# Kernel tuning notes

Hardware: AMD Instinct MI355X
Metric: run time of the kernel (lower is better)

Reference implementation:

```python
import jax, jax.numpy as jnp
import numpy as np
import math

N_EMBD = 1024
N_HEAD = 16
B, T = 4, 2048

def setup_inputs() -> dict:
    key = jax.random.key(0)
    k1, k2, k3, k4, k5 = jax.random.split(key, 5)
    C = N_EMBD
    scale_in = 1.0 / math.sqrt(C)
    x = jax.random.normal(k1, (B, T, C), dtype=jnp.float32)
    W_attn = jax.random.normal(k2, (C, 3 * C), dtype=jnp.float32) * scale_in
    b_attn = jax.random.normal(k3, (3 * C,), dtype=jnp.float32) * 0.02
    W_proj = jax.random.normal(k4, (C, C), dtype=jnp.float32) * scale_in
    b_proj = jax.random.normal(k5, (C,), dtype=jnp.float32) * 0.02
    attention_mask = jnp.ones((B, T), dtype=jnp.int32)
    return {"x": x, "W_attn": W_attn, "b_attn": b_attn,
            "W_proj": W_proj, "b_proj": b_proj,
            "attention_mask": attention_mask}

def reference(x, W_attn, b_attn, W_proj, b_proj, attention_mask):
    Bx, Tx, C = x.shape
    H = N_HEAD
    D = C // H
    qkv = x @ W_attn + b_attn                      # [B,T,3C]
    q, k, v = jnp.split(qkv, 3, axis=-1)
    # [B,H,T,D]
    q = q.reshape(Bx, Tx, H, D).transpose(0, 2, 1, 3)
    k = k.reshape(Bx, Tx, H, D).transpose(0, 2, 1, 3)
    v = v.reshape(Bx, Tx, H, D).transpose(0, 2, 1, 3)
    att = jnp.einsum('bhqd,bhkd->bhqk', q, k) * (1.0 / math.sqrt(D))
    causal = jnp.tril(jnp.ones((Tx, Tx), dtype=bool))  # [T,T]
    neg_inf = jnp.float32(-jnp.inf)
    att = jnp.where(causal[None, None, :, :], att, neg_inf)
    pad = (attention_mask != 0)[:, None, None, :]      # [B,1,1,T]
    att = jnp.where(pad, att, neg_inf)
    att = jax.nn.softmax(att, axis=-1)
    y = jnp.einsum('bhqk,bhkd->bhqd', att, v)          # [B,H,T,D]
    y = y.transpose(0, 2, 1, 3).reshape(Bx, Tx, C)
    y = y @ W_proj + b_proj
    return y
```

## Files before the change

### kernel.cpp

```cpp
#include <hip/hip_runtime.h>
#include <hip/hip_bf16.h>
#include <stdint.h>

#define B_ 4
#define T_ 2048
#define C_ 1024
#define H_ 16
#define D_ 64
#define BH_ (B_*H_)
#define M_ (B_*T_)

typedef __attribute__((ext_vector_type(8))) short short8;
typedef __attribute__((ext_vector_type(4))) float f32x4;
typedef __attribute__((ext_vector_type(16))) float f32x16;

#if __has_builtin(__builtin_amdgcn_exp2f)
#define EXP2(x) __builtin_amdgcn_exp2f(x)
#else
#define EXP2(x) exp2f(x)
#endif

#define QSCALE 0.18033688011112043f

__device__ __forceinline__ unsigned short f2bf(float f) {
  union { float f; unsigned int u; } v; v.f = f;
  unsigned int r = v.u + 0x7FFFu + ((v.u >> 16) & 1u);
  return (unsigned short)(r >> 16);
}

__device__ __forceinline__ unsigned int cvtpk_bf16(float lo, float hi) {
  unsigned int r;
  asm("v_cvt_pk_bf16_f32 %0, %1, %2" : "=v"(r) : "v"(lo), "v"(hi));
  return r;
}

__device__ __forceinline__ void gload_lds16(const void* g, void* l) {
  __builtin_amdgcn_global_load_lds(
      (__attribute__((address_space(1))) void*)g,
      (__attribute__((address_space(3))) void*)l, 16, 0, 0);
}

__global__ __launch_bounds__(256) void k_cvt(const float* __restrict__ in,
                                             unsigned short* __restrict__ out, int n) {
  int i = (blockIdx.x * 256 + threadIdx.x) * 4;
  if (i >= n) return;
  float4 v = *reinterpret_cast<const float4*>(in + i);
  union { unsigned short u[4]; unsigned long long ll; } o;
  o.u[0] = f2bf(v.x); o.u[1] = f2bf(v.y); o.u[2] = f2bf(v.z); o.u[3] = f2bf(v.w);
  *reinterpret_cast<unsigned long long*>(out + i) = o.ll;
}

__global__ __launch_bounds__(256) void k_tr(const float* __restrict__ W,
                                            unsigned short* __restrict__ Wt, int K, int N) {
  __shared__ float t[32][33];
  int n0 = blockIdx.x * 32, k0 = blockIdx.y * 32;
  int tx = threadIdx.x, ty = threadIdx.y;
  #pragma unroll
  for (int j = 0; j < 4; j++)
    t[ty + j*8][tx] = W[(size_t)(k0 + ty + j*8) * N + n0 + tx];
  __syncthreads();
  #pragma unroll
  for (int j = 0; j < 4; j++)
    Wt[(size_t)(n0 + ty + j*8) * K + k0 + tx] = f2bf(t[tx][ty + j*8]);
}

template<int QKV>
__global__ __launch_bounds__(256) void k_gemm4(const unsigned short* __restrict__ A,
                                               const unsigned short* __restrict__ Bt,
                                               const float* __restrict__ bias,
                                               void* __restrict__ outp, int N, int K) {
  __shared__ __align__(16) unsigned short Al[2][128*64];
  __shared__ __align__(16) unsigned short Bl[2][128*64];

  const int tid = threadIdx.x;
  const int lane = tid & 63, wv = tid >> 6;
  const int lg = lane >> 4, lr = lane & 15;
  const int wm = wv >> 1, wn = wv & 1;

  const int nwg = gridDim.x * gridDim.y;
  const int l = blockIdx.y * gridDim.x + blockIdx.x;
  const int wg = (l & 7) * (nwg >> 3) + (l >> 3);
  const int m0 = (wg / gridDim.x) * 128;
  const int n0 = (wg % gridDim.x) * 128;

  const int NT = K >> 6;

  auto stageA = [&](int s, int t) {
    #pragma unroll
    for (int u = 0; u < 4; ++u) {
      int gi = tid + u*256;
      int row = gi >> 3, g = gi & 7;
      gload_lds16(A + (size_t)(m0 + row) * K + t*64 + (g ^ (row & 7)) * 8,
                  (char*)Al[s] + gi*16);
    }
  };
  auto stageB = [&](int s, int t) {
    #pragma unroll
    for (int u = 0; u < 4; ++u) {
      int gi = tid + u*256;
      int row = gi >> 3, g = gi & 7;
      gload_lds16(Bt + (size_t)(n0 + row) * K + t*64 + (g ^ (row & 7)) * 8,
                  (char*)Bl[s] + gi*16);
    }
  };

  f32x4 acc[4][4];
  #pragma unroll
  for (int i = 0; i < 4; ++i)
    #pragma unroll
    for (int j = 0; j < 4; ++j) acc[i][j] = (f32x4){0.f, 0.f, 0.f, 0.f};

  stageA(0, 0); stageB(0, 0);
  asm volatile("s_waitcnt vmcnt(0)" ::: "memory");
  __builtin_amdgcn_s_barrier();

  for (int t = 0; t < NT; ++t) {
    const char* Asb = (const char*)Al[t & 1];
    const char* Bsb = (const char*)Bl[t & 1];
    const int s1 = (t & 1) ^ 1;
    const bool sn = (t + 1 < NT);
    short8 af[2][2], ag[2][2], bf[4][2];

    #pragma unroll
    for (int mf = 0; mf < 2; ++mf) {
      int row = wm*64 + mf*16 + lr; int r7 = row & 7;
      af[mf][0] = *(const short8*)(Asb + row*128 + ((lg      ^ r7) << 4));
      af[mf][1] = *(const short8*)(Asb + row*128 + (((4|lg) ^ r7) << 4));
    }
    #pragma unroll
    for (int nf = 0; nf < 4; ++nf) {
      int col = wn*64 + nf*16 + lr; int c7 = col & 7;
      bf[nf][0] = *(const short8*)(Bsb + col*128 + ((lg      ^ c7) << 4));
      bf[nf][1] = *(const short8*)(Bsb + col*128 + (((4|lg) ^ c7) << 4));
    }
    if (sn) { stageA(s1, t + 1); stageB(s1, t + 1); }
    __builtin_amdgcn_s_barrier();
    asm volatile("s_waitcnt lgkmcnt(0)" ::: "memory");
    __builtin_amdgcn_sched_barrier(0);
    __builtin_amdgcn_s_setprio(1);
    #pragma unroll
    for (int kh = 0; kh < 2; ++kh)
      #pragma unroll
      for (int mf = 0; mf < 2; ++mf)
        #pragma unroll
        for (int nf = 0; nf < 4; ++nf)
          acc[mf][nf] = __builtin_amdgcn_mfma_f32_16x16x32_bf16(
              af[mf][kh], bf[nf][kh], acc[mf][nf], 0, 0, 0);
    __builtin_amdgcn_s_setprio(0);
    __builtin_amdgcn_s_barrier();

    #pragma unroll
    for (int mf = 0; mf < 2; ++mf) {
      int row = wm*64 + (mf+2)*16 + lr; int r7 = row & 7;
      ag[mf][0] = *(const short8*)(Asb + row*128 + ((lg      ^ r7) << 4));
      ag[mf][1] = *(const short8*)(Asb + row*128 + (((4|lg) ^ r7) << 4));
    }
    __builtin_amdgcn_s_barrier();
    asm volatile("s_waitcnt lgkmcnt(0)" ::: "memory");
    __builtin_amdgcn_sched_barrier(0);
    __builtin_amdgcn_s_setprio(1);
    #pragma unroll
    for (int kh = 0; kh < 2; ++kh)
      #pragma unroll
      for (int mf = 0; mf < 2; ++mf)
        #pragma unroll
        for (int nf = 0; nf < 4; ++nf)
          acc[mf+2][nf] = __builtin_amdgcn_mfma_f32_16x16x32_bf16(
              ag[mf][kh], bf[nf][kh], acc[mf+2][nf], 0, 0, 0);
    __builtin_amdgcn_s_setprio(0);
    asm volatile("s_waitcnt vmcnt(0)" ::: "memory");
    __builtin_amdgcn_s_barrier();
  }

  if (QKV) {
    unsigned short* qb = (unsigned short*)outp;
    const size_t SZ = (size_t)BH_ * T_ * D_;
    #pragma unroll
    for (int i4 = 0; i4 < 4; ++i4) {
      int mb = m0 + wm*64 + i4*16 + lg*4;
      #pragma unroll
      for (int nf = 0; nf < 4; ++nf) {
        int n = n0 + wn*64 + nf*16 + lr;
        float bv = bias[n];
        int which = n >> 10, c = n & 1023, h = c >> 6, d = c & 63;
        if (which == 2) {
          int bb2 = mb >> 11, tt = mb & 2047;
          union { unsigned short h4[4]; unsigned long long ll; } pk;
          #pragma unroll
          for (int r = 0; r < 4; ++r) pk.h4[r] = f2bf(acc[i4][nf][r] + bv);
          unsigned short* vbase = qb + 2 * SZ;
          *reinterpret_cast<unsigned long long*>(
              &vbase[((size_t)(bb2*H_ + h)*D_ + d)*T_ + tt]) = pk.ll;
        } else {
          unsigned short* base = qb + (size_t)which * SZ;
          #pragma unroll
          for (int r = 0; r < 4; ++r) {
            int m = mb + r;
            int bb2 = m >> 11, tt = m & 2047;
            float y = acc[i4][nf][r] + bv;
            if (which == 0) y *= QSCALE;
            base[((size_t)(bb2*H_ + h)*T_ + tt)*D_ + d] = f2bf(y);
          }
        }
      }
    }
  } else {
    float* out = (float*)outp;
    #pragma unroll
    for (int i4 = 0; i4 < 4; ++i4) {
      int mb = m0 + wm*64 + i4*16 + lg*4;
      #pragma unroll
      for (int nf = 0; nf < 4; ++nf) {
        int n = n0 + wn*64 + nf*16 + lr;
        float bv = bias[n];
        #pragma unroll
        for (int r = 0; r < 4; ++r)
          out[(size_t)(mb + r)*N + n] = acc[i4][nf][r] + bv;
      }
    }
  }
}

__global__ __launch_bounds__(256, 2) void k_attn4(const unsigned short* __restrict__ Qb,
                                                  const unsigned short* __restrict__ Kb,
                                                  const unsigned short* __restrict__ Vb,
                                                  const int* __restrict__ amask,
                                                  unsigned short* __restrict__ Yb) {
  __shared__ __align__(16) char pool[65536];

  const int l = blockIdx.y * 16 + blockIdx.x;
  const int local = l >> 3;
  const int tq = 15 - (local >> 3);
  const int bh = (l & 7) * 8 + (local & 7);
  const int bb = bh >> 4, hh = bh & 15;

  const int tid = threadIdx.x;
  const int lane = tid & 63, w = tid >> 6;
  const int hi = lane >> 5, l31 = lane & 31;

  const unsigned short* Qh = Qb + (size_t)bh * (T_*D_);
  const unsigned short* Kh = Kb + (size_t)bh * (T_*D_);
  const unsigned short* Vh = Vb + (size_t)bh * (T_*D_);

  auto stage_load = [&](int i, int b, int& nm0, int& nm1) {
    const int kv0 = i << 7;
    char* base = pool + b * 32768;
    #pragma unroll
    for (int s = 0; s < 4; ++s) {
      int gi = tid + s * 256;
      int row = gi >> 3, gc = gi & 7;
      gload_lds16(Kh + (size_t)(kv0 + row)*D_ + (gc ^ (row & 7)) * 8, base + gi * 16);
    }
    #pragma unroll
    for (int s = 0; s < 4; ++s) {
      int gi = tid + s * 256;
      int d = gi >> 4, q = gi & 15;
      gload_lds16(Vh + (size_t)d*T_ + kv0 + ((q ^ (d & 15)) * 8),
                  base + 16384 + gi * 16);
    }
    nm0 = amask[bb*T_ + kv0 + lane];
    nm1 = amask[bb*T_ + kv0 + 64 + lane];
  };

  const int nT = tq + 1;
  const int qbase = tq << 7;
  const int qw = qbase + w * 32;
  const int q  = qw + l31;

  short8 qf[4];
  #pragma unroll
  for (int dt = 0; dt < 4; ++dt)
    qf[dt] = *reinterpret_cast<const short8*>(Qh + (size_t)q*D_ + dt*16 + hi*8);

  f32x16 o0, o1;
  #pragma unroll
  for (int r = 0; r < 16; ++r) { o0[r] = 0.f; o1[r] = 0.f; }
  float mr = 0.f, ls = 0.f;

  int cm0, cm1;
  stage_load(0, 0, cm0, cm1);
  __syncthreads();

  for (int i = 0; i < nT; ++i) {
    const int b = i & 1;
    const bool pf = (i + 1 < nT);
    int nm0 = 0, nm1 = 0;
    if (pf) stage_load(i + 1, b ^ 1, nm0, nm1);
    const int kv0 = i << 7;

    const unsigned short* Klb = (const unsigned short*)(pool + b * 32768);
    const char* Vtb = pool + b * 32768 + 16384;

    f32x16 st[4];
    #pragma unroll
    for (int tl = 0; tl < 4; ++tl)
      #pragma unroll
      for (int r = 0; r < 16; ++r) st[tl][r] = 0.f;
    __builtin_amdgcn_s_setprio(1);
    #pragma unroll
    for (int dt = 0; dt < 4; ++dt) {
      int gg = dt * 2 + hi;
      #pragma unroll
      for (int tl = 0; tl < 4; ++tl) {
        int ra = tl*32 + l31;
        short8 kf = *reinterpret_cast<const short8*>(Klb + ra*64 + ((gg ^ (ra & 7)) * 8));
        st[tl] = __builtin_amdgcn_mfma_f32_32x32x16_bf16(kf, qf[dt], st[tl], 0, 0, 0);
      }
    }
    __builtin_amdgcn_s_setprio(0);

    if (kv0 + 127 > qw) {
      #pragma unroll
      for (int tl = 0; tl < 4; ++tl)
        #pragma unroll
        for (int r = 0; r < 16; ++r) {
          int kvl = tl*32 + (r & 3) + 8 * (r >> 2) + 4 * hi;
          if (kv0 + kvl > q) st[tl][r] = -1e30f;
        }
    }
    unsigned long long mb0 = __ballot(cm0 != 0);
    unsigned long long mb1 = __ballot(cm1 != 0);
    if ((mb0 & mb1) != ~0ull) {
      #pragma unroll
      for (int tl = 0; tl < 4; ++tl) {
        unsigned long long mb = (tl < 2) ? mb0 : mb1;
        int sh0 = (tl & 1) * 32;
        #pragma unroll
        for (int r = 0; r < 16; ++r) {
          int kvl = (r & 3) + 8 * (r >> 2) + 4 * hi;
          if (!((mb >> (kvl + sh0)) & 1)) st[tl][r] = -1e30f;
        }
      }
    }

    float rp[8];
    #pragma unroll
    for (int r = 0; r < 8; ++r) rp[r] = 0.f;
    #pragma unroll
    for (int tl = 0; tl < 4; ++tl)
      #pragma unroll
      for (int r = 0; r < 16; ++r) {
        st[tl][r] = EXP2(st[tl][r] - mr);
        rp[r & 7] += st[tl][r];
      }
    float rs = ((rp[0] + rp[1]) + (rp[2] + rp[3])) + ((rp[4] + rp[5]) + (rp[6] + rp[7]));
    rs += __shfl_xor(rs, 32);

    unsigned int pw[4][4][2];
    #pragma unroll
    for (int tl = 0; tl < 4; ++tl)
      #pragma unroll
      for (int a = 0; a < 4; ++a) {
        pw[tl][a][0] = cvtpk_bf16(st[tl][4*a],   st[tl][4*a+1]);
        pw[tl][a][1] = cvtpk_bf16(st[tl][4*a+2], st[tl][4*a+3]);
      }

    #pragma unroll
    for (int kt = 0; kt < 8; ++kt) {
      const int t = kt >> 1, h2 = kt & 1;
      unsigned int send0 = hi ? pw[t][2*h2][0]   : pw[t][2*h2+1][0];
      unsigned int send1 = hi ? pw[t][2*h2][1]   : pw[t][2*h2+1][1];
      unsigned int own0  = hi ? pw[t][2*h2+1][0] : pw[t][2*h2][0];
      unsigned int own1  = hi ? pw[t][2*h2+1][1] : pw[t][2*h2][1];
      unsigned int recv0 = __shfl_xor(send0, 32);
      unsigned int recv1 = __shfl_xor(send1, 32);
      union { unsigned int u[4]; short8 v; } pf2;
      pf2.u[0] = hi ? recv0 : own0;
      pf2.u[1] = hi ? recv1 : own1;
      pf2.u[2] = hi ? own0  : recv0;
      pf2.u[3] = hi ? own1  : recv1;
      int gg = kt * 2 + hi;
      int dA = l31;
      short8 vf0 = *reinterpret_cast<const short8*>(Vtb + dA*256 + ((gg ^ (dA & 15)) * 16));
      int dB = 32 + l31;
      short8 vf1 = *reinterpret_cast<const short8*>(Vtb + dB*256 + ((gg ^ (dB & 15)) * 16));
      __builtin_amdgcn_s_setprio(1);
      o0 = __builtin_amdgcn_mfma_f32_32x32x16_bf16(vf0, pf2.v, o0, 0, 0, 0);
      o1 = __builtin_amdgcn_mfma_f32_32x32x16_bf16(vf1, pf2.v, o1, 0, 0, 0);
      __builtin_amdgcn_s_setprio(0);
    }

    if (__all(rs <= 65536.f)) {
      ls += rs;
    } else {
      float lgf;
      asm("v_log_f32 %0, %1" : "=v"(lgf) : "v"(rs));
      int lgi = (int)lgf + 1;
      float corr = __int_as_float((unsigned)(127 - lgi) << 23);
      mr += (float)lgi;
      ls = (ls + rs) * corr;
      #pragma unroll
      for (int r = 0; r < 16; ++r) { o0[r] *= corr; o1[r] *= corr; }
    }

    if (pf) { cm0 = nm0; cm1 = nm1; }
    __syncthreads();
  }

  float inv = 1.0f / ls;
  size_t rowbase = ((size_t)bb*T_ + q)*C_ + hh*D_;
  #pragma unroll
  for (int a = 0; a < 4; ++a) {
    union { unsigned short h[4]; unsigned long long ll; } y0, y1;
    #pragma unroll
    for (int bq = 0; bq < 4; ++bq) {
      int r = 4*a + bq;
      y0.h[bq] = f2bf(o0[r] * inv);
      y1.h[bq] = f2bf(o1[r] * inv);
    }
    int d0o = 8*a + 4*hi;
    *reinterpret_cast<unsigned long long*>(Yb + rowbase + d0o)      = y0.ll;
    *reinterpret_cast<unsigned long long*>(Yb + rowbase + 32 + d0o) = y1.ll;
  }
}

extern "C" void kernel_launch(void* const* d_in, const int* in_sizes, int n_in,
                              void* d_out, int out_size, void* d_ws, size_t ws_size,
                              hipStream_t stream) {
  const float* x      = (const float*)d_in[0];
  const float* W_attn = (const float*)d_in[1];
  const float* b_attn = (const float*)d_in[2];
  const float* W_proj = (const float*)d_in[3];
  const float* b_proj = (const float*)d_in[4];
  const int*   amask  = (const int*)d_in[5];
  float* out = (float*)d_out;

  char* ws = (char*)d_ws;
  size_t off = 0;
  auto alloc = [&](size_t bytes) { char* p = ws + off; off += (bytes + 255) & ~(size_t)255; return p; };
  unsigned short* xb   = (unsigned short*)alloc((size_t)M_ * C_ * 2);
  unsigned short* Wta  = (unsigned short*)alloc((size_t)3 * C_ * C_ * 2);
  unsigned short* Wtp  = (unsigned short*)alloc((size_t)C_ * C_ * 2);
  unsigned short* qkvb = (unsigned short*)alloc((size_t)3 * BH_ * T_ * D_ * 2);
  unsigned short* Yb   = (unsigned short*)alloc((size_t)M_ * C_ * 2);

  k_cvt<<<(M_ * C_) / 1024, 256, 0, stream>>>(x, xb, M_ * C_);
  k_tr<<<dim3(3*C_/32, C_/32), dim3(32, 8), 0, stream>>>(W_attn, Wta, C_, 3*C_);
  k_tr<<<dim3(C_/32,  C_/32),  dim3(32, 8), 0, stream>>>(W_proj, Wtp, C_, C_);

  k_gemm4<1><<<dim3(3*C_/128, M_/128), 256, 0, stream>>>(xb, Wta, b_attn, qkvb, 3*C_, C_);

  unsigned short* Qb = qkvb;
  unsigned short* Kb = qkvb + (size_t)BH_ * T_ * D_;
  unsigned short* Vb = qkvb + 2 * (size_t)BH_ * T_ * D_;
  k_attn4<<<dim3(16, BH_), 256, 0, stream>>>(Qb, Kb, Vb, amask, Yb);

  k_gemm4<0><<<dim3(C_/128, M_/128), 256, 0, stream>>>(Yb, Wtp, b_proj, out, C_, C_);
}
```

Before: 162.1 us.

## Load GEMM B operand directly from global into registers, drop B LDS staging

The GEMM kernel no longer stages the weight (B) tile through LDS. Each wave loads its B fragments straight from global memory into registers, prefetching the next K-tile after the MFMAs. The two half-step MFMA phases are merged into one, which removes several barriers and halves LDS usage. The cost is that B fragments are read redundantly by the waves sharing a column (wm=0/1), the global loads are uncoalesced 16-byte reads per lane, and register pressure rises.

```diff
diff --git a/kernel.cpp b/kernel.cpp
--- a/kernel.cpp
+++ b/kernel.cpp
@@ -70,7 +70,6 @@
                                                const float* __restrict__ bias,
                                                void* __restrict__ outp, int N, int K) {
   __shared__ __align__(16) unsigned short Al[2][128*64];
-  __shared__ __align__(16) unsigned short Bl[2][128*64];
 
   const int tid = threadIdx.x;
   const int lane = tid & 63, wv = tid >> 6;
@@ -94,13 +93,13 @@
                   (char*)Al[s] + gi*16);
     }
   };
-  auto stageB = [&](int s, int t) {
-    #pragma unroll
-    for (int u = 0; u < 4; ++u) {
-      int gi = tid + u*256;
-      int row = gi >> 3, g = gi & 7;
-      gload_lds16(Bt + (size_t)(n0 + row) * K + t*64 + (g ^ (row & 7)) * 8,
-                  (char*)Bl[s] + gi*16);
+  const unsigned short* Bw = Bt + (size_t)(n0 + wn*64 + lr) * K + lg*8;
+  auto loadB = [&](int t, short8 (&b)[4][2]) {
+    #pragma unroll
+    for (int nf = 0; nf < 4; ++nf) {
+      const unsigned short* p = Bw + (size_t)(nf*16) * K + t*64;
+      b[nf][0] = *reinterpret_cast<const short8*>(p);
+      b[nf][1] = *reinterpret_cast<const short8*>(p + 32);
     }
   };
 
@@ -110,65 +109,45 @@
     #pragma unroll
     for (int j = 0; j < 4; ++j) acc[i][j] = (f32x4){0.f, 0.f, 0.f, 0.f};
 
-  stageA(0, 0); stageB(0, 0);
+  short8 bA[4][2];
+  stageA(0, 0);
+  loadB(0, bA);
   asm volatile("s_waitcnt vmcnt(0)" ::: "memory");
   __builtin_amdgcn_s_barrier();
 
   for (int t = 0; t < NT; ++t) {
     const char* Asb = (const char*)Al[t & 1];
-    const char* Bsb = (const char*)Bl[t & 1];
     const int s1 = (t & 1) ^ 1;
     const bool sn = (t + 1 < NT);
-    short8 af[2][2], ag[2][2], bf[4][2];
-
-    #pragma unroll
-    for (int mf = 0; mf < 2; ++mf) {
+    short8 af[4][2];
+
+    #pragma unroll
+    for (int mf = 0; mf < 4; ++mf) {
       int row = wm*64 + mf*16 + lr; int r7 = row & 7;
       af[mf][0] = *(const short8*)(Asb + row*128 + ((lg      ^ r7) << 4));
       af[mf][1] = *(const short8*)(Asb + row*128 + (((4|lg) ^ r7) << 4));
     }
-    #pragma unroll
-    for (int nf = 0; nf < 4; ++nf) {
-      int col = wn*64 + nf*16 + lr; int c7 = col & 7;
-      bf[nf][0] = *(const short8*)(Bsb + col*128 + ((lg      ^ c7) << 4));
-      bf[nf][1] = *(const short8*)(Bsb + col*128 + (((4|lg) ^ c7) << 4));
-    }
-    if (sn) { stageA(s1, t + 1); stageB(s1, t + 1); }
-    __builtin_amdgcn_s_barrier();
+    if (sn) stageA(s1, t + 1);
+
     asm volatile("s_waitcnt lgkmcnt(0)" ::: "memory");
     __builtin_amdgcn_sched_barrier(0);
     __builtin_amdgcn_s_setprio(1);
     #pragma unroll
     for (int kh = 0; kh < 2; ++kh)
       #pragma unroll
-      for (int mf = 0; mf < 2; ++mf)
+      for (int mf = 0; mf < 4; ++mf)
         #pragma unroll
         for (int nf = 0; nf < 4; ++nf)
           acc[mf][nf] = __builtin_amdgcn_mfma_f32_16x16x32_bf16(
-              af[mf][kh], bf[nf][kh], acc[mf][nf], 0, 0, 0);
+              af[mf][kh], bA[nf][kh], acc[mf][nf], 0, 0, 0);
     __builtin_amdgcn_s_setprio(0);
-    __builtin_amdgcn_s_barrier();
-
-    #pragma unroll
-    for (int mf = 0; mf < 2; ++mf) {
-      int row = wm*64 + (mf+2)*16 + lr; int r7 = row & 7;
-      ag[mf][0] = *(const short8*)(Asb + row*128 + ((lg      ^ r7) << 4));
-      ag[mf][1] = *(const short8*)(Asb + row*128 + (((4|lg) ^ r7) << 4));
-    }
-    __builtin_amdgcn_s_barrier();
-    asm volatile("s_waitcnt lgkmcnt(0)" ::: "memory");
-    __builtin_amdgcn_sched_barrier(0);
-    __builtin_amdgcn_s_setprio(1);
-    #pragma unroll
-    for (int kh = 0; kh < 2; ++kh)
-      #pragma unroll
-      for (int mf = 0; mf < 2; ++mf)
-        #pragma unroll
-        for (int nf = 0; nf < 4; ++nf)
-          acc[mf+2][nf] = __builtin_amdgcn_mfma_f32_16x16x32_bf16(
-              ag[mf][kh], bf[nf][kh], acc[mf+2][nf], 0, 0, 0);
-    __builtin_amdgcn_s_setprio(0);
-    asm volatile("s_waitcnt vmcnt(0)" ::: "memory");
+
+    if (sn) {
+      loadB(t + 1, bA);
+      asm volatile("s_waitcnt vmcnt(8)" ::: "memory");
+    } else {
+      asm volatile("s_waitcnt vmcnt(0)" ::: "memory");
+    }
     __builtin_amdgcn_s_barrier();
   }
 
```

Result: slower. 227.3 us (+40.2%).
